# Kernel optimization log

Measured on AMD Instinct MI355X. Metric: run time of the kernel, lower is better.

Reference implementation:

```python
import jax, jax.numpy as jnp
import numpy as np

POOL = 8  # kernel_size = [8, 1]: pool factor 8 along H (for *_H) and along W (for *_W)

def _pool_h(x, k):
    B, C, H, W = x.shape
    return x.reshape(B, C, H // k, k, W).mean(axis=3)  # (B,C,H/k,W)

def _pool_w(x, k):
    B, C, H, W = x.shape
    return x.reshape(B, C, H, W // k, k).mean(axis=4)  # (B,C,H,W/k)

def setup_inputs() -> dict:
    key = jax.random.key(0)
    k1, k2 = jax.random.split(key)
    shape = (8, 256, 128, 128)
    return {
        "tensor1": jax.random.normal(k1, shape, dtype=jnp.float32),
        "tensor2": jax.random.normal(k2, shape, dtype=jnp.float32),
    }

def reference(tensor1, tensor2):
    B, C, H, W = tensor1.shape
    kH, kW = H // POOL, W // POOL
    # pooled keys (from tensor1) and values (from tensor2)
    key_H = _pool_h(tensor1, POOL)    # (B,C,kH,W)
    key_W = _pool_w(tensor1, POOL)    # (B,C,H,kW)
    val_H = _pool_h(tensor2, POOL)    # (B,C,kH,W)
    val_W = _pool_w(tensor2, POOL)    # (B,C,H,kW)
    # criss-cross energies: contract over (c, w) for H-branch, (c, h) for W-branch
    energy_H = jnp.einsum('bchw,bckw->bhk', tensor2, key_H).reshape(B, H * kH)
    energy_W = jnp.einsum('bchw,bchk->bwk', tensor2, key_W).reshape(B, W * kW)
    energy = jnp.concatenate([energy_H, energy_W], axis=-1)
    # global (all-element) min-max normalization, then softmax over concat axis
    e_min, e_max = energy.min(), energy.max()
    energy = (energy - e_min) / (e_max - e_min)
    concate = jax.nn.softmax(energy, axis=-1)
    att_H = concate[:, : H * kH].reshape(B, H, kH)
    att_W = concate[:, H * kH :].reshape(B, W, kW)
    out_H = jnp.einsum('bckw,bhk->bchw', val_H, att_H)
    out_W = jnp.einsum('bchk,bwk->bchw', val_W, att_W)
    gamma = jnp.float32(0.5)
    return gamma * (out_H + out_W) + tensor2
```

## Files before the change

### kernel.cpp

```cpp
#include <hip/hip_runtime.h>
#include <cstddef>

#define CC 256
#define HH 128
#define WW 128
#define HW (HH*WW)

typedef __attribute__((ext_vector_type(8))) short short8v;
typedef __attribute__((ext_vector_type(4))) float float4v;

__device__ __forceinline__ short f2bf(float x) {
    unsigned u = __float_as_uint(x);
    u += 0x7FFFu + ((u >> 16) & 1u);
    return (short)(u >> 16);
}
__device__ __forceinline__ float4 add4(float4 a, float4 b) {
    float4 r; r.x=a.x+b.x; r.y=a.y+b.y; r.z=a.z+b.z; r.w=a.w+b.w; return r;
}
__device__ __forceinline__ float4 scale4(float4 a, float s) {
    float4 r; r.x=a.x*s; r.y=a.y*s; r.z=a.z*s; r.w=a.w*s; return r;
}
__device__ __forceinline__ float4 shflx4(float4 v, int m) {
    float4 r;
    r.x = __shfl_xor(v.x, m); r.y = __shfl_xor(v.y, m);
    r.z = __shfl_xor(v.z, m); r.w = __shfl_xor(v.w, m);
    return r;
}
__device__ __forceinline__ float hsum4(float4 v) { return v.x+v.y+v.z+v.w; }

#define GLD4(dst, addr, OFFSTR) \
    asm volatile("global_load_dwordx4 %0, %1, off offset:" OFFSTR \
                 : "=v"(dst) : "v"(addr) : "memory")

#define WAITVM(NSTR) { asm volatile("s_waitcnt vmcnt(" NSTR ")" ::: "memory"); \
                       __builtin_amdgcn_sched_barrier(0); }
#define BAR_LDS { asm volatile("s_waitcnt lgkmcnt(0)" ::: "memory"); \
                  __builtin_amdgcn_sched_barrier(0); \
                  __builtin_amdgcn_s_barrier(); }

__global__ __launch_bounds__(512, 4) void fused_pool_energy(
    const float* __restrict__ t1, const float* __restrict__ t2,
    unsigned short* __restrict__ valHT, unsigned short* __restrict__ valWbf,
    float* __restrict__ PH, float* __restrict__ PW)
{
    __shared__ __align__(16) short t2lds[64*128];
    __shared__ __align__(16) short t2T  [128*64];
    __shared__ __align__(16) short kH   [16*128];
    __shared__ __align__(16) short kWT  [16*128];

    const int bid = blockIdx.x;
    const int b   = bid & 7;
    const int c   = bid >> 3;
    const int tid = threadIdx.x;
    const int l   = tid & 63;
    const int wv  = tid >> 6;
    const int q   = tid & 31;
    const int g   = tid >> 5;
    const int bc  = b*CC + c;
    const size_t cbase = (size_t)bc * HW;
    const float4* t1c = (const float4*)(t1 + cbase);
    const float4* t2c = (const float4*)(t2 + cbase);

    const float4* ap = t1c + g*256 + q;
    const float4* cp = t2c + g*128 + q;
    const float4* dp = cp + 2048;
    float4 aR[8], cR[4], dR[4];
    GLD4(aR[0], ap, "0");    GLD4(aR[1], ap, "512");
    GLD4(aR[2], ap, "1024"); GLD4(aR[3], ap, "1536");
    GLD4(aR[4], ap, "2048"); GLD4(aR[5], ap, "2560");
    GLD4(aR[6], ap, "3072"); GLD4(aR[7], ap, "3584");
    GLD4(cR[0], cp, "0");    GLD4(cR[1], cp, "512");
    GLD4(cR[2], cp, "1024"); GLD4(cR[3], cp, "1536");
    GLD4(dR[0], dp, "0");    GLD4(dR[1], dp, "512");
    GLD4(dR[2], dp, "1024"); GLD4(dR[3], dp, "1536");

    WAITVM("8");
    {
        float4 s = add4(add4(add4(aR[0],aR[1]), add4(aR[2],aR[3])),
                        add4(add4(aR[4],aR[5]), add4(aR[6],aR[7])));
        float4 m4 = scale4(s, 0.125f);
        short4 p; p.x=f2bf(m4.x); p.y=f2bf(m4.y); p.z=f2bf(m4.z); p.w=f2bf(m4.w);
        *(short4*)&kH[g*128 + ((q*4) ^ ((g&7)<<3))] = p;
        const int kw = q >> 1;
        const int sw = (kw & 7) << 3;
        #pragma unroll
        for (int r = 0; r < 8; ++r) {
            float rs = hsum4(aR[r]);
            rs += __shfl_xor(rs, 1);
            if ((l & 1) == 0)
                kWT[kw*128 + ((g*8+r) ^ sw)] = f2bf(rs * 0.125f);
        }
    }
    BAR_LDS;

    float4v accH = {0.f,0.f,0.f,0.f};
    float4v accW = {0.f,0.f,0.f,0.f};

    WAITVM("0");

    #pragma unroll
    for (int half = 0; half < 2; ++half) {
        float4 x0, x1, x2, x3;
        if (half == 0) { x0=cR[0]; x1=cR[1]; x2=cR[2]; x3=cR[3]; }
        else           { x0=dR[0]; x1=dR[1]; x2=dR[2]; x3=dR[3]; }

        {
            float4 sB = add4(add4(x0,x1), add4(x2,x3));
            float4 f8 = add4(sB, shflx4(sB, 32));
            if (l < 32) {
                const int k = half*8 + wv;
                const size_t vb = (size_t)bc * 2048;
                valHT[vb + (q*4+0)*16 + k] = (unsigned short)f2bf(f8.x * 0.125f);
                valHT[vb + (q*4+1)*16 + k] = (unsigned short)f2bf(f8.y * 0.125f);
                valHT[vb + (q*4+2)*16 + k] = (unsigned short)f2bf(f8.z * 0.125f);
                valHT[vb + (q*4+3)*16 + k] = (unsigned short)f2bf(f8.w * 0.125f);
            }
        }
        {
            const int kw = q >> 1;
            float r0 = hsum4(x0), r1 = hsum4(x1), r2 = hsum4(x2), r3 = hsum4(x3);
            r0 += __shfl_xor(r0, 1); r1 += __shfl_xor(r1, 1);
            r2 += __shfl_xor(r2, 1); r3 += __shfl_xor(r3, 1);
            if ((l & 1) == 0) {
                const size_t vb = (size_t)bc*2048 + (size_t)(half*64 + g*4)*16 + kw;
                valWbf[vb +  0] = (unsigned short)f2bf(r0 * 0.125f);
                valWbf[vb + 16] = (unsigned short)f2bf(r1 * 0.125f);
                valWbf[vb + 32] = (unsigned short)f2bf(r2 * 0.125f);
                valWbf[vb + 48] = (unsigned short)f2bf(r3 * 0.125f);
            }
        }
        short4 s0, s1, s2, s3;
        s0.x=f2bf(x0.x); s0.y=f2bf(x0.y); s0.z=f2bf(x0.z); s0.w=f2bf(x0.w);
        s1.x=f2bf(x1.x); s1.y=f2bf(x1.y); s1.z=f2bf(x1.z); s1.w=f2bf(x1.w);
        s2.x=f2bf(x2.x); s2.y=f2bf(x2.y); s2.z=f2bf(x2.z); s2.w=f2bf(x2.w);
        s3.x=f2bf(x3.x); s3.y=f2bf(x3.y); s3.z=f2bf(x3.z); s3.w=f2bf(x3.w);
        {
            const int hl0 = g*4;
            *(short4*)&t2lds[(hl0+0)*128 + ((q*4) ^ (((hl0+0)&7)<<3))] = s0;
            *(short4*)&t2lds[(hl0+1)*128 + ((q*4) ^ (((hl0+1)&7)<<3))] = s1;
            *(short4*)&t2lds[(hl0+2)*128 + ((q*4) ^ (((hl0+2)&7)<<3))] = s2;
            *(short4*)&t2lds[(hl0+3)*128 + ((q*4) ^ (((hl0+3)&7)<<3))] = s3;
            const int swt = (q & 7) << 3;
            const int hb  = hl0 ^ swt;
            short4 p;
            p.x=s0.x; p.y=s1.x; p.z=s2.x; p.w=s3.x;
            *(short4*)&t2T[(q*4+0)*64 + hb] = p;
            p.x=s0.y; p.y=s1.y; p.z=s2.y; p.w=s3.y;
            *(short4*)&t2T[(q*4+1)*64 + hb] = p;
            p.x=s0.z; p.y=s1.z; p.z=s2.z; p.w=s3.z;
            *(short4*)&t2T[(q*4+2)*64 + hb] = p;
            p.x=s0.w; p.y=s1.w; p.z=s2.w; p.w=s3.w;
            *(short4*)&t2T[(q*4+3)*64 + hb] = p;
        }
        BAR_LDS;

        if ((wv >> 2) == half) {
            const int hl = (wv & 3)*16 + (l & 15);
            const int kb = l & 15;
            #pragma unroll
            for (int ws2 = 0; ws2 < 4; ++ws2) {
                const int wb = ws2*32 + (l>>4)*8;
                short8v A = *(const short8v*)&t2lds[hl*128 + (wb ^ ((hl&7)<<3))];
                short8v B = *(const short8v*)&kH  [kb*128 + (wb ^ ((kb&7)<<3))];
                accH = __builtin_amdgcn_mfma_f32_16x16x32_bf16(A, B, accH, 0, 0, 0);
            }
        }
        {
            const int kb = l & 15;
            const int w  = wv*16 + (l & 15);
            const int swt = ((w >> 2) & 7) << 3;
            #pragma unroll
            for (int hs = 0; hs < 2; ++hs) {
                const int hloc = hs*32 + (l>>4)*8;
                const int hg   = half*64 + hloc;
                short8v A = *(const short8v*)&kWT[kb*128 + (hg ^ ((kb&7)<<3))];
                short8v B = *(const short8v*)&t2T[w*64   + (hloc ^ swt)];
                accW = __builtin_amdgcn_mfma_f32_16x16x32_bf16(A, B, accW, 0, 0, 0);
            }
        }
        BAR_LDS;
    }

    {
        const size_t pb = (size_t)bc * 2048;
        #pragma unroll
        for (int r = 0; r < 4; ++r) {
            const int h = wv*16 + (l>>4)*4 + r;
            PH[pb + h*16 + (l&15)] = accH[r];
            const int k = (l>>4)*4 + r;
            PW[pb + k*128 + wv*16 + (l&15)] = accW[r];
        }
    }
}

__global__ __launch_bounds__(256) void energy_reduce(
    const float* __restrict__ PH, const float* __restrict__ PW,
    float* __restrict__ energy, float* __restrict__ bmin, float* __restrict__ bmax)
{
    const int bidx = blockIdx.x;
    const int tid  = threadIdx.x;
    const int ol   = tid & 63, qd = tid >> 6;
    const int o    = bidx*64 + ol;
    __shared__ float red[4][64];

    const int isW = o >> 14;
    const int oo  = o & 16383;
    const int b   = oo >> 11, i = oo & 2047;
    const float* P = (isW ? PW : PH) + (size_t)b*256*2048 + i;
    float s = 0.f;
    #pragma unroll 8
    for (int j = 0; j < 64; ++j) s += P[(size_t)(qd*64 + j)*2048];
    red[qd][ol] = s;
    __syncthreads();

    if (tid < 64) {
        float v = red[0][tid] + red[1][tid] + red[2][tid] + red[3][tid];
        const int o2 = bidx*64 + tid;
        const int oo2 = o2 & 16383;
        const int b2 = oo2 >> 11, i2 = oo2 & 2047;
        const size_t dst = (o2 >> 14)
            ? ((size_t)b2*4096 + 2048 + (size_t)(i2 & 127)*16 + (i2 >> 7))
            : ((size_t)b2*4096 + i2);
        energy[dst] = v;
        float mn = v, mx = v;
        #pragma unroll
        for (int sft = 32; sft > 0; sft >>= 1) {
            mn = fminf(mn, __shfl_xor(mn, sft));
            mx = fmaxf(mx, __shfl_xor(mx, sft));
        }
        if (tid == 0) { bmin[bidx] = mn; bmax[bidx] = mx; }
    }
}

__global__ __launch_bounds__(1024) void softmax_kernel(
    const float* __restrict__ energy, const float* __restrict__ bmin,
    const float* __restrict__ bmax,
    unsigned short* __restrict__ aHbf, unsigned short* __restrict__ aWbf)
{
    const int b = blockIdx.x, tid = threadIdx.x;
    const int lane = tid & 63, wid = tid >> 6;
    __shared__ float smn[16], smx[16], sred[16], bc2[2];

    float mn = 3.0e38f, mx = -3.0e38f;
    if (tid < 512) { mn = bmin[tid]; mx = bmax[tid]; }
    #pragma unroll
    for (int s = 32; s > 0; s >>= 1) {
        mn = fminf(mn, __shfl_xor(mn, s));
        mx = fmaxf(mx, __shfl_xor(mx, s));
    }
    if (lane == 0) { smn[wid] = mn; smx[wid] = mx; }
    __syncthreads();
    if (tid == 0) {
        float a = smn[0], m = smx[0];
        #pragma unroll
        for (int i = 1; i < 16; ++i) { a = fminf(a, smn[i]); m = fmaxf(m, smx[i]); }
        bc2[0] = a; bc2[1] = m;
    }
    __syncthreads();
    const float gmn = bc2[0];
    const float inv = 1.0f / (bc2[1] - gmn);

    float4 v = ((const float4*)energy)[b*1024 + tid];
    float4 e;
    e.x = __expf((v.x - gmn) * inv);
    e.y = __expf((v.y - gmn) * inv);
    e.z = __expf((v.z - gmn) * inv);
    e.w = __expf((v.w - gmn) * inv);
    float loc = e.x + e.y + e.z + e.w;
    #pragma unroll
    for (int s = 32; s > 0; s >>= 1) loc += __shfl_down(loc, s);
    if (lane == 0) sred[wid] = loc;
    __syncthreads();
    if (tid == 0) {
        float a = 0.f;
        #pragma unroll
        for (int j = 0; j < 16; ++j) a += sred[j];
        bc2[0] = 1.0f / a;
    }
    __syncthreads();
    const float r = bc2[0];
    short4 p;
    p.x = f2bf(e.x * r); p.y = f2bf(e.y * r);
    p.z = f2bf(e.z * r); p.w = f2bf(e.w * r);
    if (tid < 512)
        *(short4*)&aHbf[(size_t)b*2048 + tid*4] = p;
    else
        *(short4*)&aWbf[(size_t)b*2048 + (tid-512)*4] = p;
}

__global__ __launch_bounds__(256) void out_kernel(
    const float* __restrict__ t2,
    const unsigned short* __restrict__ valHT,
    const unsigned short* __restrict__ valWbf,
    const unsigned short* __restrict__ aHbf,
    const unsigned short* __restrict__ aWbf,
    float* __restrict__ out)
{
    const int bid = blockIdx.x;
    const int b = bid & 7, c = bid >> 3;
    const int bc = b*CC + c;
    const int tid = threadIdx.x;
    const int l  = tid & 63;
    const int wv = tid >> 6;
    const int ln = l & 15;
    const int q4 = l >> 4;
    const size_t tb = (size_t)bc * HW;

    const unsigned short* vHT = valHT  + (size_t)bc*2048;
    const unsigned short* vW  = valWbf + (size_t)bc*2048;
    const unsigned short* aH  = aHbf + (size_t)b*2048;
    const unsigned short* aW  = aWbf + (size_t)b*2048;

    short8v Bf[8];
    {
        const unsigned short* src = (q4 < 2) ? vHT : aW;
        #pragma unroll
        for (int tw = 0; tw < 8; ++tw)
            Bf[tw] = *(const short8v*)&src[(tw*16 + ln)*16 + (q4 & 1)*8];
    }

    #pragma unroll
    for (int t = 0; t < 2; ++t) {
        const int th = wv*2 + t;
        const unsigned short* asrc = (q4 < 2) ? aH : vW;
        short8v Af = *(const short8v*)&asrc[(th*16 + ln)*16 + (q4 & 1)*8];
        #pragma unroll
        for (int tw = 0; tw < 8; ++tw) {
            float4v acc = {0.f,0.f,0.f,0.f};
            acc = __builtin_amdgcn_mfma_f32_16x16x32_bf16(Af, Bf[tw], acc, 0, 0, 0);
            const size_t base = tb + (size_t)(th*16 + q4*4)*128 + tw*16 + ln;
            #pragma unroll
            for (int r = 0; r < 4; ++r) {
                const float tv = t2[base + (size_t)r*128];
                out[base + (size_t)r*128] = fmaf(0.5f, acc[r], tv);
            }
        }
    }
}

extern "C" void kernel_launch(void* const* d_in, const int* in_sizes, int n_in,
                              void* d_out, int out_size, void* d_ws, size_t ws_size,
                              hipStream_t stream)
{
    const float* t1 = (const float*)d_in[0];
    const float* t2 = (const float*)d_in[1];
    float* out = (float*)d_out;
    char*  ws  = (char*)d_ws;

    unsigned short* valHT  = (unsigned short*)ws;
    unsigned short* valWbf = (unsigned short*)(ws + ((size_t)8 << 20));
    float* energy = (float*)(ws + ((size_t)16 << 20));
    float* bmin   = energy + 32768;
    float* bmax   = bmin + 512;
    unsigned short* aHbf = (unsigned short*)(ws + ((size_t)17 << 20));
    unsigned short* aWbf = aHbf + 8*2048;

    float* PH = out;
    float* PW = out + (size_t)4194304;

    hipLaunchKernelGGL(fused_pool_energy, dim3(2048), dim3(512), 0, stream,
                       t1, t2, valHT, valWbf, PH, PW);
    hipLaunchKernelGGL(energy_reduce, dim3(512), dim3(256), 0, stream,
                       PH, PW, energy, bmin, bmax);
    hipLaunchKernelGGL(softmax_kernel, dim3(8), dim3(1024), 0, stream,
                       energy, bmin, bmax, aHbf, aWbf);
    hipLaunchKernelGGL(out_kernel, dim3(2048), dim3(256), 0, stream,
                       t2, valHT, valWbf, aHbf, aWbf, out);
}
```

Before: 137.4 us.

## Process four channels per block with prefetched loads and in-register accumulation

The fused pool/energy kernel now handles four consecutive channels per block (512 blocks instead of 2048). While the current channel is being processed, it software-pipelines the global loads for the next one, and it accumulates the MFMA partial energies across channels in registers. This cuts the partial-energy buffers written to global memory by four, so the reduce kernel reads 64 partials per output instead of 256. The cost is fewer blocks (less parallelism and latency hiding across the GPU) and more register pressure from the prefetch buffers.

After: 144.0 us. +4.8%, slower.

```diff
diff --git a/kernel.cpp b/kernel.cpp
--- a/kernel.cpp
+++ b/kernel.cpp
@@ -38,6 +38,117 @@
                   __builtin_amdgcn_sched_barrier(0); \
                   __builtin_amdgcn_s_barrier(); }
 
+#define ISSUE_A(P) { GLD4(aR[0], P, "0");    GLD4(aR[1], P, "512");  \
+                     GLD4(aR[2], P, "1024"); GLD4(aR[3], P, "1536"); \
+                     GLD4(aR[4], P, "2048"); GLD4(aR[5], P, "2560"); \
+                     GLD4(aR[6], P, "3072"); GLD4(aR[7], P, "3584"); }
+#define ISSUE_C(P) { GLD4(cR[0], P, "0");    GLD4(cR[1], P, "512");  \
+                     GLD4(cR[2], P, "1024"); GLD4(cR[3], P, "1536"); }
+#define ISSUE_D(P) { GLD4(dR[0], P, "0");    GLD4(dR[1], P, "512");  \
+                     GLD4(dR[2], P, "1024"); GLD4(dR[3], P, "1536"); }
+
+__device__ __forceinline__ void phaseA(
+    const float4* aR, short* kH, short* kWT, int l, int q, int g)
+{
+    float4 s = add4(add4(add4(aR[0],aR[1]), add4(aR[2],aR[3])),
+                    add4(add4(aR[4],aR[5]), add4(aR[6],aR[7])));
+    float4 m4 = scale4(s, 0.125f);
+    short4 p; p.x=f2bf(m4.x); p.y=f2bf(m4.y); p.z=f2bf(m4.z); p.w=f2bf(m4.w);
+    *(short4*)&kH[g*128 + ((q*4) ^ ((g&7)<<3))] = p;
+    const int kw = q >> 1;
+    const int sw = (kw & 7) << 3;
+    #pragma unroll
+    for (int r = 0; r < 8; ++r) {
+        float rs = hsum4(aR[r]);
+        rs += __shfl_xor(rs, 1);
+        if ((l & 1) == 0)
+            kWT[kw*128 + ((g*8+r) ^ sw)] = f2bf(rs * 0.125f);
+    }
+}
+
+__device__ __forceinline__ void process_half(
+    float4 x0, float4 x1, float4 x2, float4 x3, int half, int bc,
+    unsigned short* valHT, unsigned short* valWbf,
+    short* t2lds, short* t2T, int l, int q, int g, int wv)
+{
+    {
+        float4 sB = add4(add4(x0,x1), add4(x2,x3));
+        float4 f8 = add4(sB, shflx4(sB, 32));
+        const int k = half*8 + wv;
+        const size_t vb = (size_t)bc * 2048;
+        if (l < 32) {
+            valHT[vb + (q*4+0)*16 + k] = (unsigned short)f2bf(f8.x * 0.125f);
+            valHT[vb + (q*4+1)*16 + k] = (unsigned short)f2bf(f8.y * 0.125f);
+            valHT[vb + (q*4+2)*16 + k] = (unsigned short)f2bf(f8.z * 0.125f);
+            valHT[vb + (q*4+3)*16 + k] = (unsigned short)f2bf(f8.w * 0.125f);
+        }
+    }
+    {
+        const int kw = q >> 1;
+        float r0 = hsum4(x0), r1 = hsum4(x1), r2 = hsum4(x2), r3 = hsum4(x3);
+        r0 += __shfl_xor(r0, 1); r1 += __shfl_xor(r1, 1);
+        r2 += __shfl_xor(r2, 1); r3 += __shfl_xor(r3, 1);
+        if ((l & 1) == 0) {
+            const size_t vb = (size_t)bc*2048 + (size_t)(half*64 + g*4)*16 + kw;
+            valWbf[vb +  0] = (unsigned short)f2bf(r0 * 0.125f);
+            valWbf[vb + 16] = (unsigned short)f2bf(r1 * 0.125f);
+            valWbf[vb + 32] = (unsigned short)f2bf(r2 * 0.125f);
+            valWbf[vb + 48] = (unsigned short)f2bf(r3 * 0.125f);
+        }
+    }
+    short4 s0, s1, s2, s3;
+    s0.x=f2bf(x0.x); s0.y=f2bf(x0.y); s0.z=f2bf(x0.z); s0.w=f2bf(x0.w);
+    s1.x=f2bf(x1.x); s1.y=f2bf(x1.y); s1.z=f2bf(x1.z); s1.w=f2bf(x1.w);
+    s2.x=f2bf(x2.x); s2.y=f2bf(x2.y); s2.z=f2bf(x2.z); s2.w=f2bf(x2.w);
+    s3.x=f2bf(x3.x); s3.y=f2bf(x3.y); s3.z=f2bf(x3.z); s3.w=f2bf(x3.w);
+    const int hl0 = g*4;
+    *(short4*)&t2lds[(hl0+0)*128 + ((q*4) ^ (((hl0+0)&7)<<3))] = s0;
+    *(short4*)&t2lds[(hl0+1)*128 + ((q*4) ^ (((hl0+1)&7)<<3))] = s1;
+    *(short4*)&t2lds[(hl0+2)*128 + ((q*4) ^ (((hl0+2)&7)<<3))] = s2;
+    *(short4*)&t2lds[(hl0+3)*128 + ((q*4) ^ (((hl0+3)&7)<<3))] = s3;
+    const int swt = (q & 7) << 3;
+    const int hb  = hl0 ^ swt;
+    short4 p;
+    p.x=s0.x; p.y=s1.x; p.z=s2.x; p.w=s3.x;
+    *(short4*)&t2T[(q*4+0)*64 + hb] = p;
+    p.x=s0.y; p.y=s1.y; p.z=s2.y; p.w=s3.y;
+    *(short4*)&t2T[(q*4+1)*64 + hb] = p;
+    p.x=s0.z; p.y=s1.z; p.z=s2.z; p.w=s3.z;
+    *(short4*)&t2T[(q*4+2)*64 + hb] = p;
+    p.x=s0.w; p.y=s1.w; p.z=s2.w; p.w=s3.w;
+    *(short4*)&t2T[(q*4+3)*64 + hb] = p;
+}
+
+__device__ __forceinline__ void mfma_half(
+    const short* t2lds, const short* t2T, const short* kH, const short* kWT,
+    int wv, int l, int half, float4v& accH, float4v& accW)
+{
+    if ((wv >> 2) == half) {
+        const int hl = (wv & 3)*16 + (l & 15);
+        const int kb = l & 15;
+        #pragma unroll
+        for (int ws2 = 0; ws2 < 4; ++ws2) {
+            const int wb = ws2*32 + (l>>4)*8;
+            short8v A = *(const short8v*)&t2lds[hl*128 + (wb ^ ((hl&7)<<3))];
+            short8v B = *(const short8v*)&kH  [kb*128 + (wb ^ ((kb&7)<<3))];
+            accH = __builtin_amdgcn_mfma_f32_16x16x32_bf16(A, B, accH, 0, 0, 0);
+        }
+    }
+    {
+        const int kb = l & 15;
+        const int w  = wv*16 + (l & 15);
+        const int swt = ((w >> 2) & 7) << 3;
+        #pragma unroll
+        for (int hs = 0; hs < 2; ++hs) {
+            const int hloc = hs*32 + (l>>4)*8;
+            const int hg   = half*64 + hloc;
+            short8v A = *(const short8v*)&kWT[kb*128 + (hg ^ ((kb&7)<<3))];
+            short8v B = *(const short8v*)&t2T[w*64   + (hloc ^ swt)];
+            accW = __builtin_amdgcn_mfma_f32_16x16x32_bf16(A, B, accW, 0, 0, 0);
+        }
+    }
+}
+
 __global__ __launch_bounds__(512, 4) void fused_pool_energy(
     const float* __restrict__ t1, const float* __restrict__ t2,
     unsigned short* __restrict__ valHT, unsigned short* __restrict__ valWbf,
@@ -50,145 +161,63 @@
 
     const int bid = blockIdx.x;
     const int b   = bid & 7;
-    const int c   = bid >> 3;
+    const int grp = bid >> 3;
+    const int c0  = grp * 4;
     const int tid = threadIdx.x;
     const int l   = tid & 63;
     const int wv  = tid >> 6;
     const int q   = tid & 31;
     const int g   = tid >> 5;
-    const int bc  = b*CC + c;
-    const size_t cbase = (size_t)bc * HW;
-    const float4* t1c = (const float4*)(t1 + cbase);
-    const float4* t2c = (const float4*)(t2 + cbase);
-
-    const float4* ap = t1c + g*256 + q;
-    const float4* cp = t2c + g*128 + q;
-    const float4* dp = cp + 2048;
+
+    const float4* ap0 = (const float4*)(t1 + ((size_t)b*CC + c0)*HW) + g*256 + q;
+    const float4* cp0 = (const float4*)(t2 + ((size_t)b*CC + c0)*HW) + g*128 + q;
+
     float4 aR[8], cR[4], dR[4];
-    GLD4(aR[0], ap, "0");    GLD4(aR[1], ap, "512");
-    GLD4(aR[2], ap, "1024"); GLD4(aR[3], ap, "1536");
-    GLD4(aR[4], ap, "2048"); GLD4(aR[5], ap, "2560");
-    GLD4(aR[6], ap, "3072"); GLD4(aR[7], ap, "3584");
-    GLD4(cR[0], cp, "0");    GLD4(cR[1], cp, "512");
-    GLD4(cR[2], cp, "1024"); GLD4(cR[3], cp, "1536");
-    GLD4(dR[0], dp, "0");    GLD4(dR[1], dp, "512");
-    GLD4(dR[2], dp, "1024"); GLD4(dR[3], dp, "1536");
-
-    WAITVM("8");
-    {
-        float4 s = add4(add4(add4(aR[0],aR[1]), add4(aR[2],aR[3])),
-                        add4(add4(aR[4],aR[5]), add4(aR[6],aR[7])));
-        float4 m4 = scale4(s, 0.125f);
-        short4 p; p.x=f2bf(m4.x); p.y=f2bf(m4.y); p.z=f2bf(m4.z); p.w=f2bf(m4.w);
-        *(short4*)&kH[g*128 + ((q*4) ^ ((g&7)<<3))] = p;
-        const int kw = q >> 1;
-        const int sw = (kw & 7) << 3;
-        #pragma unroll
-        for (int r = 0; r < 8; ++r) {
-            float rs = hsum4(aR[r]);
-            rs += __shfl_xor(rs, 1);
-            if ((l & 1) == 0)
-                kWT[kw*128 + ((g*8+r) ^ sw)] = f2bf(rs * 0.125f);
-        }
-    }
-    BAR_LDS;
-
     float4v accH = {0.f,0.f,0.f,0.f};
     float4v accW = {0.f,0.f,0.f,0.f};
 
-    WAITVM("0");
-
-    #pragma unroll
-    for (int half = 0; half < 2; ++half) {
-        float4 x0, x1, x2, x3;
-        if (half == 0) { x0=cR[0]; x1=cR[1]; x2=cR[2]; x3=cR[3]; }
-        else           { x0=dR[0]; x1=dR[1]; x2=dR[2]; x3=dR[3]; }
-
-        {
-            float4 sB = add4(add4(x0,x1), add4(x2,x3));
-            float4 f8 = add4(sB, shflx4(sB, 32));
-            if (l < 32) {
-                const int k = half*8 + wv;
-                const size_t vb = (size_t)bc * 2048;
-                valHT[vb + (q*4+0)*16 + k] = (unsigned short)f2bf(f8.x * 0.125f);
-                valHT[vb + (q*4+1)*16 + k] = (unsigned short)f2bf(f8.y * 0.125f);
-                valHT[vb + (q*4+2)*16 + k] = (unsigned short)f2bf(f8.z * 0.125f);
-                valHT[vb + (q*4+3)*16 + k] = (unsigned short)f2bf(f8.w * 0.125f);
-            }
-        }
-        {
-            const int kw = q >> 1;
-            float r0 = hsum4(x0), r1 = hsum4(x1), r2 = hsum4(x2), r3 = hsum4(x3);
-            r0 += __shfl_xor(r0, 1); r1 += __shfl_xor(r1, 1);
-            r2 += __shfl_xor(r2, 1); r3 += __shfl_xor(r3, 1);
-            if ((l & 1) == 0) {
-                const size_t vb = (size_t)bc*2048 + (size_t)(half*64 + g*4)*16 + kw;
-                valWbf[vb +  0] = (unsigned short)f2bf(r0 * 0.125f);
-                valWbf[vb + 16] = (unsigned short)f2bf(r1 * 0.125f);
-                valWbf[vb + 32] = (unsigned short)f2bf(r2 * 0.125f);
-                valWbf[vb + 48] = (unsigned short)f2bf(r3 * 0.125f);
-            }
-        }
-        short4 s0, s1, s2, s3;
-        s0.x=f2bf(x0.x); s0.y=f2bf(x0.y); s0.z=f2bf(x0.z); s0.w=f2bf(x0.w);
-        s1.x=f2bf(x1.x); s1.y=f2bf(x1.y); s1.z=f2bf(x1.z); s1.w=f2bf(x1.w);
-        s2.x=f2bf(x2.x); s2.y=f2bf(x2.y); s2.z=f2bf(x2.z); s2.w=f2bf(x2.w);
-        s3.x=f2bf(x3.x); s3.y=f2bf(x3.y); s3.z=f2bf(x3.z); s3.w=f2bf(x3.w);
-        {
-            const int hl0 = g*4;
-            *(short4*)&t2lds[(hl0+0)*128 + ((q*4) ^ (((hl0+0)&7)<<3))] = s0;
-            *(short4*)&t2lds[(hl0+1)*128 + ((q*4) ^ (((hl0+1)&7)<<3))] = s1;
-            *(short4*)&t2lds[(hl0+2)*128 + ((q*4) ^ (((hl0+2)&7)<<3))] = s2;
-            *(short4*)&t2lds[(hl0+3)*128 + ((q*4) ^ (((hl0+3)&7)<<3))] = s3;
-            const int swt = (q & 7) << 3;
-            const int hb  = hl0 ^ swt;
-            short4 p;
-            p.x=s0.x; p.y=s1.x; p.z=s2.x; p.w=s3.x;
-            *(short4*)&t2T[(q*4+0)*64 + hb] = p;
-            p.x=s0.y; p.y=s1.y; p.z=s2.y; p.w=s3.y;
-            *(short4*)&t2T[(q*4+1)*64 + hb] = p;
-            p.x=s0.z; p.y=s1.z; p.z=s2.z; p.w=s3.z;
-            *(short4*)&t2T[(q*4+2)*64 + hb] = p;
-            p.x=s0.w; p.y=s1.w; p.z=s2.w; p.w=s3.w;
-            *(short4*)&t2T[(q*4+3)*64 + hb] = p;
-        }
+    ISSUE_A(ap0); ISSUE_C(cp0); ISSUE_D(cp0 + 2048);
+    WAITVM("8");
+    phaseA(aR, kH, kWT, l, q, g);
+    BAR_LDS;
+    ISSUE_A(ap0 + 4096);
+
+    #pragma unroll
+    for (int ci = 0; ci < 4; ++ci) {
+        const int bc = b*CC + c0 + ci;
+        const float4* cpi = cp0 + ci*4096;
+
+        if (ci < 3) WAITVM("12") else WAITVM("4");
+        process_half(cR[0],cR[1],cR[2],cR[3], 0, bc, valHT, valWbf,
+                     t2lds, t2T, l, q, g, wv);
         BAR_LDS;
-
-        if ((wv >> 2) == half) {
-            const int hl = (wv & 3)*16 + (l & 15);
-            const int kb = l & 15;
-            #pragma unroll
-            for (int ws2 = 0; ws2 < 4; ++ws2) {
-                const int wb = ws2*32 + (l>>4)*8;
-                short8v A = *(const short8v*)&t2lds[hl*128 + (wb ^ ((hl&7)<<3))];
-                short8v B = *(const short8v*)&kH  [kb*128 + (wb ^ ((kb&7)<<3))];
-                accH = __builtin_amdgcn_mfma_f32_16x16x32_bf16(A, B, accH, 0, 0, 0);
-            }
-        }
-        {
-            const int kb = l & 15;
-            const int w  = wv*16 + (l & 15);
-            const int swt = ((w >> 2) & 7) << 3;
-            #pragma unroll
-            for (int hs = 0; hs < 2; ++hs) {
-                const int hloc = hs*32 + (l>>4)*8;
-                const int hg   = half*64 + hloc;
-                short8v A = *(const short8v*)&kWT[kb*128 + (hg ^ ((kb&7)<<3))];
-                short8v B = *(const short8v*)&t2T[w*64   + (hloc ^ swt)];
-                accW = __builtin_amdgcn_mfma_f32_16x16x32_bf16(A, B, accW, 0, 0, 0);
-            }
-        }
+        mfma_half(t2lds, t2T, kH, kWT, wv, l, 0, accH, accW);
         BAR_LDS;
-    }
-
-    {
-        const size_t pb = (size_t)bc * 2048;
+
+        if (ci < 3) WAITVM("16") else WAITVM("8");
+        process_half(dR[0],dR[1],dR[2],dR[3], 1, bc, valHT, valWbf,
+                     t2lds, t2T, l, q, g, wv);
+        BAR_LDS;
+        if (ci < 3) { ISSUE_C(cpi + 4096); ISSUE_D(cpi + 4096 + 2048); }
+        mfma_half(t2lds, t2T, kH, kWT, wv, l, 1, accH, accW);
+        BAR_LDS;
+
+        if (ci < 3) {
+            WAITVM("24");
+            phaseA(aR, kH, kWT, l, q, g);
+            BAR_LDS;
+            if (ci < 2) ISSUE_A(ap0 + (ci+2)*4096);
+        }
+    }
+
+    {
+        const size_t pb = (size_t)bid * 2048;
         #pragma unroll
         for (int r = 0; r < 4; ++r) {
-            const int h = wv*16 + (l>>4)*4 + r;
-            PH[pb + h*16 + (l&15)] = accH[r];
+            const int h = (wv>>2)*64 + (wv&3)*16 + (l>>4)*4 + r;
+            PH[pb + (size_t)h*16 + (l&15)] = accH[r];
             const int k = (l>>4)*4 + r;
-            PW[pb + k*128 + wv*16 + (l&15)] = accW[r];
+            PW[pb + (size_t)k*128 + wv*16 + (l&15)] = accW[r];
         }
     }
 }
@@ -206,10 +235,11 @@
     const int isW = o >> 14;
     const int oo  = o & 16383;
     const int b   = oo >> 11, i = oo & 2047;
-    const float* P = (isW ? PW : PH) + (size_t)b*256*2048 + i;
+    const float* P = (isW ? PW : PH) + (size_t)b*2048 + i;
     float s = 0.f;
-    #pragma unroll 8
-    for (int j = 0; j < 64; ++j) s += P[(size_t)(qd*64 + j)*2048];
+    #pragma unroll
+    for (int j = 0; j < 16; ++j)
+        s += P[(size_t)((qd*16 + j)*8) * 2048];
     red[qd][ol] = s;
     __syncthreads();
 
@@ -356,9 +386,9 @@
     unsigned short* aWbf = aHbf + 8*2048;
 
     float* PH = out;
-    float* PW = out + (size_t)4194304;
-
-    hipLaunchKernelGGL(fused_pool_energy, dim3(2048), dim3(512), 0, stream,
+    float* PW = out + (size_t)1048576;
+
+    hipLaunchKernelGGL(fused_pool_energy, dim3(512), dim3(512), 0, stream,
                        t1, t2, valHT, valWbf, PH, PW);
     hipLaunchKernelGGL(energy_reduce, dim3(512), dim3(256), 0, stream,
                        PH, PW, energy, bmin, bmax);
```
